# Optimization experiments

Measured on AMD Instinct MI355X. Metric: run time of the kernel, lower is better.

The kernel has to match this reference:

```python
import jax, jax.numpy as jnp
import numpy as np


def setup_inputs() -> dict:
    key = jax.random.key(0)
    x = jax.random.normal(key, (256, 128, 2048), dtype=jnp.float32)
    return {"x": x}


def reference(x) -> jnp.ndarray:
    # x: (batch, channels, time)
    # 1) average reference: subtract mean across channels per (batch, time)
    x = x - jnp.mean(x, axis=1, keepdims=True)
    # 2) channel-wise zscore: mean/std over time axis per (batch, channel)
    mean = jnp.mean(x, axis=2, keepdims=True)
    std = jnp.std(x, axis=2, keepdims=True)  # population std (ddof=0), matches np.std
    std = jnp.where(std == 0, jnp.ones_like(std), std)
    return (x - mean) / std
```

## Files before the change

kernel.cpp:

```cpp
#include <hip/hip_runtime.h>


#define B 256
#define C 128
#define T 2048

__launch_bounds__(256)
__global__ void mu_kernel(const float* __restrict__ x, float* __restrict__ mu) {
    const int b = blockIdx.y;
    const int t0 = blockIdx.x * 256;
    const int tid = threadIdx.x;
    const int wave = tid >> 6;
    const int lane = tid & 63;

    const float4* __restrict__ xp =
        reinterpret_cast<const float4*>(x + ((size_t)b * C + wave * 32) * T + t0);

    float4 acc = make_float4(0.f, 0.f, 0.f, 0.f);
    #pragma unroll 8
    for (int k = 0; k < 32; ++k) {
        float4 v = xp[(size_t)k * (T / 4) + lane];
        acc.x += v.x; acc.y += v.y; acc.z += v.z; acc.w += v.w;
    }

    __shared__ float4 part[4][64];
    part[wave][lane] = acc;
    __syncthreads();

    if (wave == 0) {
        float4 p0 = part[0][lane], p1 = part[1][lane];
        float4 p2 = part[2][lane], p3 = part[3][lane];
        const float invC = 1.0f / (float)C;
        float4 s;
        s.x = (p0.x + p1.x + p2.x + p3.x) * invC;
        s.y = (p0.y + p1.y + p2.y + p3.y) * invC;
        s.z = (p0.z + p1.z + p2.z + p3.z) * invC;
        s.w = (p0.w + p1.w + p2.w + p3.w) * invC;
        reinterpret_cast<float4*>(mu + (size_t)b * T + t0)[lane] = s;
    }
}

__launch_bounds__(256)
__global__ void zscore_kernel(const float* __restrict__ x,
                              const float* __restrict__ mu,
                              float* __restrict__ out) {
    const int bc = blockIdx.x;
    const int b = bc >> 7;
    const int tid = threadIdx.x;
    const int wave = tid >> 6;
    const int lane = tid & 63;

    const float4* __restrict__ xc = reinterpret_cast<const float4*>(x + (size_t)bc * T);
    const float4* __restrict__ mc = reinterpret_cast<const float4*>(mu + (size_t)b * T);

    float4 v0 = xc[tid];
    float4 v1 = xc[tid + 256];
    float4 m0 = mc[tid];
    float4 m1 = mc[tid + 256];

    float4 y0, y1;
    y0.x = v0.x - m0.x; y0.y = v0.y - m0.y; y0.z = v0.z - m0.z; y0.w = v0.w - m0.w;
    y1.x = v1.x - m1.x; y1.y = v1.y - m1.y; y1.z = v1.z - m1.z; y1.w = v1.w - m1.w;

    float sum = ((y0.x + y0.y) + (y0.z + y0.w)) + ((y1.x + y1.y) + (y1.z + y1.w));
    float sq  = ((y0.x * y0.x + y0.y * y0.y) + (y0.z * y0.z + y0.w * y0.w))
              + ((y1.x * y1.x + y1.y * y1.y) + (y1.z * y1.z + y1.w * y1.w));

    #pragma unroll
    for (int off = 32; off > 0; off >>= 1) {
        sum += __shfl_xor(sum, off, 64);
        sq  += __shfl_xor(sq,  off, 64);
    }

    __shared__ float2 wsum[4];
    if (lane == 0) wsum[wave] = make_float2(sum, sq);
    __syncthreads();

    float2 a0 = wsum[0], a1 = wsum[1], a2 = wsum[2], a3 = wsum[3];
    float tsum = (a0.x + a1.x) + (a2.x + a3.x);
    float tsq  = (a0.y + a1.y) + (a2.y + a3.y);

    const float invT = 1.0f / (float)T;
    float mean = tsum * invT;
    float var = tsq * invT - mean * mean;
    var = fmaxf(var, 0.f);
    float sd = sqrtf(var);
    float inv = (sd == 0.f) ? 1.0f : 1.0f / sd;

    float4* __restrict__ oc = reinterpret_cast<float4*>(out + (size_t)bc * T);
    float4 o0, o1;
    o0.x = (y0.x - mean) * inv; o0.y = (y0.y - mean) * inv;
    o0.z = (y0.z - mean) * inv; o0.w = (y0.w - mean) * inv;
    o1.x = (y1.x - mean) * inv; o1.y = (y1.y - mean) * inv;
    o1.z = (y1.z - mean) * inv; o1.w = (y1.w - mean) * inv;
    oc[tid] = o0;
    oc[tid + 256] = o1;
}

extern "C" void kernel_launch(void* const* d_in, const int* in_sizes, int n_in,
                              void* d_out, int out_size, void* d_ws, size_t ws_size,
                              hipStream_t stream) {
    const float* x = (const float*)d_in[0];
    float* out = (float*)d_out;
    float* mu = (float*)d_ws;

    dim3 gridA(T / 256, B);
    mu_kernel<<<gridA, 256, 0, stream>>>(x, mu);
    zscore_kernel<<<B * C, 256, 0, stream>>>(x, mu, out);
}
```

Before: 477.0 us.

## Fuse channel-mean and z-score kernels into one per-batch block

Replaces the two-kernel pipeline with a single kernel where each 1024-thread block handles one batch: it computes per-time channel means into shared memory, then normalizes each channel. This removes the global mu round trip and the second launch, and aims to get the re-read of x from cache by walking channels in reverse order. Output uses nontemporal stores so it does not pollute cache. The risk is low occupancy and serialization, with one large block per CU and a barrier between phases.

```diff
diff --git a/kernel.cpp b/kernel.cpp
--- a/kernel.cpp
+++ b/kernel.cpp
@@ -4,97 +4,93 @@
 #define B 256
 #define C 128
 #define T 2048
+#define T4 (T / 4)
 
-__launch_bounds__(256)
-__global__ void mu_kernel(const float* __restrict__ x, float* __restrict__ mu) {
-    const int b = blockIdx.y;
-    const int t0 = blockIdx.x * 256;
+typedef float f4 __attribute__((ext_vector_type(4)));
+
+__launch_bounds__(1024)
+__global__ void eeg_fused(const float* __restrict__ x, float* __restrict__ out) {
+    const int b = blockIdx.x;
     const int tid = threadIdx.x;
+
+    __shared__ float4 mu4[T4];
+    __shared__ float4 part[T4];
+
+    const float4* __restrict__ xb =
+        reinterpret_cast<const float4*>(x) + (size_t)b * C * T4;
+    float4* __restrict__ ob =
+        reinterpret_cast<float4*>(out) + (size_t)b * C * T4;
+
+    {
+        const int t4 = tid & (T4 - 1);
+        const int g  = tid >> 9;
+        const float4* __restrict__ xp = xb + (size_t)(g * 64) * T4 + t4;
+
+        float4 acc = make_float4(0.f, 0.f, 0.f, 0.f);
+        #pragma unroll 8
+        for (int k = 0; k < 64; ++k) {
+            float4 v = xp[(size_t)k * T4];
+            acc.x += v.x; acc.y += v.y; acc.z += v.z; acc.w += v.w;
+        }
+        if (g) part[t4] = acc;
+        else   mu4[t4]  = acc;
+        __syncthreads();
+        if (!g) {
+            const float invC = 1.0f / (float)C;
+            float4 p = part[t4];
+            float4 m = mu4[t4];
+            m.x = (m.x + p.x) * invC;
+            m.y = (m.y + p.y) * invC;
+            m.z = (m.z + p.z) * invC;
+            m.w = (m.w + p.w) * invC;
+            mu4[t4] = m;
+        }
+        __syncthreads();
+    }
+
     const int wave = tid >> 6;
     const int lane = tid & 63;
+    const float invT = 1.0f / (float)T;
 
-    const float4* __restrict__ xp =
-        reinterpret_cast<const float4*>(x + ((size_t)b * C + wave * 32) * T + t0);
+    for (int cc = wave; cc < C; cc += 16) {
+        const int c = (C - 1) - cc;
+        const float4* __restrict__ xc = xb + (size_t)c * T4;
 
-    float4 acc = make_float4(0.f, 0.f, 0.f, 0.f);
-    #pragma unroll 8
-    for (int k = 0; k < 32; ++k) {
-        float4 v = xp[(size_t)k * (T / 4) + lane];
-        acc.x += v.x; acc.y += v.y; acc.z += v.z; acc.w += v.w;
+        float4 y[8];
+        float sum = 0.f, sq = 0.f;
+        #pragma unroll
+        for (int j = 0; j < 8; ++j) {
+            float4 v = xc[lane + j * 64];
+            float4 m = mu4[lane + j * 64];
+            y[j].x = v.x - m.x; y[j].y = v.y - m.y;
+            y[j].z = v.z - m.z; y[j].w = v.w - m.w;
+            sum += (y[j].x + y[j].y) + (y[j].z + y[j].w);
+            sq  += (y[j].x * y[j].x + y[j].y * y[j].y)
+                 + (y[j].z * y[j].z + y[j].w * y[j].w);
+        }
+
+        #pragma unroll
+        for (int off = 32; off > 0; off >>= 1) {
+            sum += __shfl_xor(sum, off, 64);
+            sq  += __shfl_xor(sq,  off, 64);
+        }
+
+        float mean = sum * invT;
+        float var  = fmaxf(sq * invT - mean * mean, 0.f);
+        float sd   = sqrtf(var);
+        float inv  = (sd == 0.f) ? 1.0f : 1.0f / sd;
+
+        float4* __restrict__ oc = ob + (size_t)c * T4;
+        #pragma unroll
+        for (int j = 0; j < 8; ++j) {
+            f4 o = { (y[j].x - mean) * inv,
+                     (y[j].y - mean) * inv,
+                     (y[j].z - mean) * inv,
+                     (y[j].w - mean) * inv };
+            __builtin_nontemporal_store(
+                o, reinterpret_cast<f4*>(oc + lane + j * 64));
+        }
     }
-
-    __shared__ float4 part[4][64];
-    part[wave][lane] = acc;
-    __syncthreads();
-
-    if (wave == 0) {
-        float4 p0 = part[0][lane], p1 = part[1][lane];
-        float4 p2 = part[2][lane], p3 = part[3][lane];
-        const float invC = 1.0f / (float)C;
-        float4 s;
-        s.x = (p0.x + p1.x + p2.x + p3.x) * invC;
-        s.y = (p0.y + p1.y + p2.y + p3.y) * invC;
-        s.z = (p0.z + p1.z + p2.z + p3.z) * invC;
-        s.w = (p0.w + p1.w + p2.w + p3.w) * invC;
-        reinterpret_cast<float4*>(mu + (size_t)b * T + t0)[lane] = s;
-    }
-}
-
-__launch_bounds__(256)
-__global__ void zscore_kernel(const float* __restrict__ x,
-                              const float* __restrict__ mu,
-                              float* __restrict__ out) {
-    const int bc = blockIdx.x;
-    const int b = bc >> 7;
-    const int tid = threadIdx.x;
-    const int wave = tid >> 6;
-    const int lane = tid & 63;
-
-    const float4* __restrict__ xc = reinterpret_cast<const float4*>(x + (size_t)bc * T);
-    const float4* __restrict__ mc = reinterpret_cast<const float4*>(mu + (size_t)b * T);
-
-    float4 v0 = xc[tid];
-    float4 v1 = xc[tid + 256];
-    float4 m0 = mc[tid];
-    float4 m1 = mc[tid + 256];
-
-    float4 y0, y1;
-    y0.x = v0.x - m0.x; y0.y = v0.y - m0.y; y0.z = v0.z - m0.z; y0.w = v0.w - m0.w;
-    y1.x = v1.x - m1.x; y1.y = v1.y - m1.y; y1.z = v1.z - m1.z; y1.w = v1.w - m1.w;
-
-    float sum = ((y0.x + y0.y) + (y0.z + y0.w)) + ((y1.x + y1.y) + (y1.z + y1.w));
-    float sq  = ((y0.x * y0.x + y0.y * y0.y) + (y0.z * y0.z + y0.w * y0.w))
-              + ((y1.x * y1.x + y1.y * y1.y) + (y1.z * y1.z + y1.w * y1.w));
-
-    #pragma unroll
-    for (int off = 32; off > 0; off >>= 1) {
-        sum += __shfl_xor(sum, off, 64);
-        sq  += __shfl_xor(sq,  off, 64);
-    }
-
-    __shared__ float2 wsum[4];
-    if (lane == 0) wsum[wave] = make_float2(sum, sq);
-    __syncthreads();
-
-    float2 a0 = wsum[0], a1 = wsum[1], a2 = wsum[2], a3 = wsum[3];
-    float tsum = (a0.x + a1.x) + (a2.x + a3.x);
-    float tsq  = (a0.y + a1.y) + (a2.y + a3.y);
-
-    const float invT = 1.0f / (float)T;
-    float mean = tsum * invT;
-    float var = tsq * invT - mean * mean;
-    var = fmaxf(var, 0.f);
-    float sd = sqrtf(var);
-    float inv = (sd == 0.f) ? 1.0f : 1.0f / sd;
-
-    float4* __restrict__ oc = reinterpret_cast<float4*>(out + (size_t)bc * T);
-    float4 o0, o1;
-    o0.x = (y0.x - mean) * inv; o0.y = (y0.y - mean) * inv;
-    o0.z = (y0.z - mean) * inv; o0.w = (y0.w - mean) * inv;
-    o1.x = (y1.x - mean) * inv; o1.y = (y1.y - mean) * inv;
-    o1.z = (y1.z - mean) * inv; o1.w = (y1.w - mean) * inv;
-    oc[tid] = o0;
-    oc[tid + 256] = o1;
 }
 
 extern "C" void kernel_launch(void* const* d_in, const int* in_sizes, int n_in,
@@ -102,9 +98,7 @@
                               hipStream_t stream) {
     const float* x = (const float*)d_in[0];
     float* out = (float*)d_out;
-    float* mu = (float*)d_ws;
+    (void)d_ws; (void)ws_size;
 
-    dim3 gridA(T / 256, B);
-    mu_kernel<<<gridA, 256, 0, stream>>>(x, mu);
-    zscore_kernel<<<B * C, 256, 0, stream>>>(x, mu, out);
+    eeg_fused<<<B, 1024, 0, stream>>>(x, out);
 }
```

After: 465.8 us. -2.4%, faster.
